# Optimization experiments

Hardware: AMD Instinct MI355X
Metric: run time of the kernel (lower is better)

The kernel has to match this reference:

```python
import jax, jax.numpy as jnp
import numpy as np

B, N, K, DIN, DM, DOUT = 4, 4096, 16, 256, 256, 256


def setup_inputs() -> dict:
    key = jax.random.key(0)
    ks = jax.random.split(key, 14)
    s = lambda k, shape: (jax.random.normal(k, shape, jnp.float32) * 0.02)
    return dict(
        xyz=jax.random.normal(ks[0], (B, N, 3), jnp.float32),
        features=jax.random.normal(ks[1], (B, N, DIN), jnp.float32),
        fc_delta_w1=s(ks[2], (3, DM)), fc_delta_b1=jnp.zeros((DM,), jnp.float32),
        fc_delta_w2=s(ks[3], (DM, DM)), fc_delta_b2=jnp.zeros((DM,), jnp.float32),
        fc1_w=s(ks[4], (DIN, DM)), fc1_b=jnp.zeros((DM,), jnp.float32),
        wq=s(ks[5], (DM, DM)), wk=s(ks[6], (DM, DM)), wv=s(ks[7], (DM, DM)),
        fc_gamma_w1=s(ks[8], (DM, DM)), fc_gamma_b1=jnp.zeros((DM,), jnp.float32),
        fc_gamma_w2=s(ks[9], (DM, DM)), fc_gamma_b2=jnp.zeros((DM,), jnp.float32),
        fc2_w=s(ks[10], (DM, DOUT)), fc2_b=jnp.zeros((DOUT,), jnp.float32),
        sc_w=s(ks[11], (DIN, DOUT)), sc_b=jnp.zeros((DOUT,), jnp.float32),
    )


def reference(xyz, features, fc_delta_w1, fc_delta_b1, fc_delta_w2, fc_delta_b2,
              fc1_w, fc1_b, wq, wk, wv, fc_gamma_w1, fc_gamma_b1,
              fc_gamma_w2, fc_gamma_b2, fc2_w, fc2_b, sc_w, sc_b):
    # kNN via squared euclidean distances (same ordering as cdist topk)
    x2 = jnp.sum(xyz * xyz, axis=-1)                                   # (B,N)
    d2 = x2[:, :, None] + x2[:, None, :] - 2.0 * jnp.einsum('bnd,bmd->bnm', xyz, xyz)
    knn_idx = jax.lax.top_k(-d2, K)[1]                                 # (B,N,K)

    gather = jax.vmap(lambda a, i: a[i])                               # per-batch gather
    knn_xyz = gather(xyz, knn_idx)                                     # (B,N,K,3)

    # positional encoding MLP on relative coordinates
    rel = xyz[:, :, None, :] - knn_xyz                                 # (B,N,K,3)
    pos_enc = jax.nn.relu(rel @ fc_delta_w1 + fc_delta_b1) @ fc_delta_w2 + fc_delta_b2

    shortcut = features
    f = features @ fc1_w + fc1_b                                       # (B,N,DM)
    knn_f = gather(f, knn_idx)                                         # (B,N,K,DM)

    q = f @ wq                                                         # (B,N,DM)
    k_ = knn_f @ wk                                                    # (B,N,K,DM)
    v = knn_f @ wv                                                     # (B,N,K,DM)

    a = q[:, :, None, :] - k_ + pos_enc                                # (B,N,K,DM)
    a = jax.nn.relu(a @ fc_gamma_w1 + fc_gamma_b1) @ fc_gamma_w2 + fc_gamma_b2
    attn = jax.nn.softmax(a / np.float32(np.sqrt(DM)), axis=-2)        # softmax over K

    res = jnp.einsum('bnkf,bnkf->bnf', attn, v + pos_enc)              # (B,N,DM)
    return res @ fc2_w + fc2_b + shortcut @ sc_w + sc_b                # (B,N,DOUT)
```

## Files before the change

### kernel.cpp

```cpp
#include <hip/hip_runtime.h>
#include <hip/hip_bf16.h>
#include <math.h>

typedef __attribute__((ext_vector_type(8))) short bf16x8;
typedef __attribute__((ext_vector_type(4))) float f32x4;
typedef __attribute__((ext_vector_type(4))) short s16x4;
typedef unsigned int u32;
typedef unsigned long long u64;

#define NBATCH 4
#define NPTS   4096
#define NTOT   (NBATCH*NPTS)
#define NROWS  (NTOT*16)

__device__ __forceinline__ float bf2f(unsigned short h){
  unsigned int u = ((unsigned int)h) << 16;
  return __builtin_bit_cast(float, u);
}
__device__ __forceinline__ unsigned short f2bf(float f){
  unsigned int u = __builtin_bit_cast(unsigned int, f);
  u += 0x7FFFu + ((u >> 16) & 1u);
  return (unsigned short)(u >> 16);
}
__device__ __forceinline__ unsigned short f2bfh(float f){
  return __bfloat16_as_ushort(__float2bfloat16(f));
}

#define MFMA(a,b,c) __builtin_amdgcn_mfma_f32_16x16x32_bf16((a),(b),(c),0,0,0)

typedef u32 __attribute__((address_space(1))) gas_u32;
typedef u32 __attribute__((address_space(3))) las_u32;
__device__ __forceinline__ void gl_lds16(const void* g, void* l){
  __builtin_amdgcn_global_load_lds((const gas_u32*)g, (las_u32*)l, 16, 0, 0);
}

__device__ __forceinline__ void wfence(){
  asm volatile("s_waitcnt lgkmcnt(0)" ::: "memory");
  __builtin_amdgcn_sched_barrier(0);
}

__global__ __launch_bounds__(256) void k_convert(const float* __restrict__ x,
                                                 unsigned short* __restrict__ xb, int n){
  int i = (blockIdx.x * 256 + threadIdx.x) * 4;
  if (i < n){
    float4 v = *(const float4*)(x + i);
    s16x4 o;
    o[0] = (short)f2bf(v.x); o[1] = (short)f2bf(v.y);
    o[2] = (short)f2bf(v.z); o[3] = (short)f2bf(v.w);
    *(s16x4*)(xb + i) = o;
  }
}

__global__ __launch_bounds__(256) void k_xyzw(const float* __restrict__ xyz,
                                              float4* __restrict__ xyzw){
  int i = blockIdx.x * 256 + threadIdx.x;
  float x = xyz[i*3], y = xyz[i*3+1], z = xyz[i*3+2];
  xyzw[i] = make_float4(x, y, z, x*x + y*y + z*z);
}

__global__ __launch_bounds__(256) void k_prep_mats(
    const float* __restrict__ scw, const float* __restrict__ g2,
    const float* __restrict__ fc2, const float* __restrict__ W2,
    const float* __restrict__ scb,
    unsigned short* __restrict__ qkv2T, unsigned short* __restrict__ g2sT,
    unsigned short* __restrict__ fc2T, unsigned short* __restrict__ BposT,
    float* __restrict__ cvec){
  int c = blockIdx.x, d = threadIdx.x;
  qkv2T[(768+c)*256 + d] = f2bf(scw[d*256 + c]);
  g2sT[c*256 + d]        = f2bf(g2[d*256 + c] * 0.0625f);
  fc2T[c*256 + d]        = f2bf(fc2[d*256 + c]);
  BposT[(256+c)*256 + d] = f2bf(W2[d*256 + c]);
  if (d == 0) cvec[768 + c] = scb[c];
}

__global__ __launch_bounds__(256) void k_prep_gemm(
    const float* __restrict__ wq, const float* __restrict__ wk,
    const float* __restrict__ g1, const float* __restrict__ W2,
    const float* __restrict__ b2d, const float* __restrict__ gb1,
    unsigned short* __restrict__ tmpWq, unsigned short* __restrict__ tmpWk,
    unsigned short* __restrict__ BposT, float* __restrict__ c1){
  int c = threadIdx.x, bid = blockIdx.x;
  if (bid < 256){
    int d = bid; float acc = 0.f;
    for (int e=0;e<256;e++) acc += wq[d*256+e]*g1[e*256+c];
    tmpWq[c*256 + d] = f2bf(acc);
  } else if (bid < 512){
    int d = bid-256; float acc = 0.f;
    for (int e=0;e<256;e++) acc += wk[d*256+e]*g1[e*256+c];
    tmpWk[c*256 + d] = f2bf(acc);
  } else if (bid < 768){
    int d = bid-512; float acc = 0.f;
    for (int e=0;e<256;e++) acc += W2[d*256+e]*g1[e*256+c];
    BposT[c*256 + d] = f2bf(acc);
  } else {
    float acc = 0.f;
    for (int e=0;e<256;e++) acc += b2d[e]*g1[e*256+c];
    c1[c] = acc + gb1[c];
  }
}

__global__ __launch_bounds__(256) void k_prep_gemm2(
    const float* __restrict__ fc1w, const float* __restrict__ fc1b,
    const float* __restrict__ wv,
    const unsigned short* __restrict__ tmpWq, const unsigned short* __restrict__ tmpWk,
    unsigned short* __restrict__ qkv2T, float* __restrict__ cvec){
  int c = threadIdx.x, bid = blockIdx.x;
  if (bid < 256){
    int d = bid; float acc = 0.f;
    for (int e=0;e<256;e++) acc += fc1w[d*256+e]*bf2f(tmpWq[c*256+e]);
    qkv2T[c*256 + d] = f2bf(acc);
  } else if (bid < 512){
    int d = bid-256; float acc = 0.f;
    for (int e=0;e<256;e++) acc += fc1w[d*256+e]*bf2f(tmpWk[c*256+e]);
    qkv2T[(256+c)*256 + d] = f2bf(acc);
  } else if (bid < 768){
    int d = bid-512; float acc = 0.f;
    for (int e=0;e<256;e++) acc += fc1w[d*256+e]*wv[e*256+c];
    qkv2T[(512+c)*256 + d] = f2bf(acc);
  } else {
    float aq=0.f, ak=0.f, av=0.f;
    for (int e=0;e<256;e++){
      float fb = fc1b[e];
      aq += fb*bf2f(tmpWq[c*256+e]);
      ak += fb*bf2f(tmpWk[c*256+e]);
      av += fb*wv[e*256+c];
    }
    cvec[c] = aq; cvec[256+c] = ak; cvec[512+c] = av;
  }
}

__device__ __forceinline__ u32 fmap(float d){
  u32 u = __builtin_bit_cast(u32, d);
  return ((int)u < 0) ? ~u : (u | 0x80000000u);
}

__device__ __forceinline__ void find_thresh(const int* hist, int lane, int need,
                                            int* e_out, int* c_out){
  int h0 = hist[lane*4], h1 = hist[lane*4+1], h2 = hist[lane*4+2], h3 = hist[lane*4+3];
  int ps = h0 + h1 + h2 + h3;
  int incl = ps;
  #pragma unroll
  for (int d = 1; d < 64; d <<= 1){
    int tv = __shfl_up(incl, d, 64);
    if (lane >= d) incl += tv;
  }
  int excl = incl - ps;
  int b0 = excl, b1 = excl + h0, b2 = b1 + h1, b3 = b2 + h2;
  bool f0 = (b0 < need) && (b0 + h0 >= need);
  bool f1 = (b1 < need) && (b1 + h1 >= need);
  bool f2 = (b2 < need) && (b2 + h2 >= need);
  bool f3 = (b3 < need) && (b3 + h3 >= need);
  int e_loc = f0 ? lane*4 : f1 ? lane*4+1 : f2 ? lane*4+2 : lane*4+3;
  int c_loc = f0 ? b0 : f1 ? b1 : f2 ? b2 : b3;
  u64 mk = __ballot(f0 | f1 | f2 | f3);
  int wl = __ffsll(mk) - 1;
  *e_out = __shfl(e_loc, wl, 64);
  *c_out = __shfl(c_loc, wl, 64);
}

__device__ __forceinline__ void find_thresh4(const int* hA, int lane, int need,
                                             int* e_out, int* c_out){
  int h[4];
  #pragma unroll
  for (int j=0;j<4;j++){
    int bin = lane*4+j;
    h[j] = hA[bin]
         + hA[256 + ((bin+8)&255)]
         + hA[512 + ((bin+16)&255)]
         + hA[768 + ((bin+24)&255)];
  }
  int ps = h[0] + h[1] + h[2] + h[3];
  int incl = ps;
  #pragma unroll
  for (int d = 1; d < 64; d <<= 1){
    int tv = __shfl_up(incl, d, 64);
    if (lane >= d) incl += tv;
  }
  int excl = incl - ps;
  int b0 = excl, b1 = excl + h[0], b2 = b1 + h[1], b3 = b2 + h[2];
  bool f0 = (b0 < need) && (b0 + h[0] >= need);
  bool f1 = (b1 < need) && (b1 + h[1] >= need);
  bool f2 = (b2 < need) && (b2 + h[2] >= need);
  bool f3 = (b3 < need) && (b3 + h[3] >= need);
  int e_loc = f0 ? lane*4 : f1 ? lane*4+1 : f2 ? lane*4+2 : lane*4+3;
  int c_loc = f0 ? b0 : f1 ? b1 : f2 ? b2 : b3;
  u64 mk = __ballot(f0 | f1 | f2 | f3);
  int wl = __ffsll(mk) - 1;
  *e_out = __shfl(e_loc, wl, 64);
  *c_out = __shfl(c_loc, wl, 64);
}

__global__ __launch_bounds__(256) void k_knn(const float4* __restrict__ xyzw,
                                             int* __restrict__ gidxbuf,
                                             float4* __restrict__ relbuf){
  __shared__ int histA[4][1024];
  __shared__ int histB[4][256];

  int t = threadIdx.x, lane = t & 63, wv = t >> 6;
  int widx = blockIdx.x * 4 + wv;
  int b = widx >> 12, n = widx & 4095;
  const float4* xb = xyzw + (size_t)b * NPTS;
  float4 P = xb[n];
  float x2n = P.w;
  int* hA = histA[wv]; int* hB = histB[wv];

  #pragma unroll
  for (int j = 0; j < 16; j++) hA[lane*16+j] = 0;
  #pragma unroll
  for (int j = 0; j < 4; j++)  hB[lane*4+j] = 0;
  wfence();

  int cp = lane >> 4;
  int cpoff = cp*256, cprot = cp*8;

  for (int it = 0; it < 64; it += 2){
    float4 Q0 = xb[it*64 + lane];
    float4 Q1 = xb[it*64 + 64 + lane];
    float d0 = x2n + Q0.w - 2.0f*(P.x*Q0.x + P.y*Q0.y + P.z*Q0.z);
    float d1 = x2n + Q1.w - 2.0f*(P.x*Q1.x + P.y*Q1.y + P.z*Q1.z);
    int b0 = (int)(fmap(d0) >> 24), b1 = (int)(fmap(d1) >> 24);
    atomicAdd(&hA[cpoff + ((b0 + cprot)&255)], 1);
    atomicAdd(&hA[cpoff + ((b1 + cprot)&255)], 1);
  }
  wfence();
  int e1, c0dummy;
  find_thresh4(hA, lane, 16, &e1, &c0dummy);
  wfence();

  u32* lstE_u = (u32*)&hA[0];
  int* lstE_m = &hA[128];
  u32* lstT_u = (u32*)&hA[256];
  int* lstT_m = &hA[320];

  int base = 0, Lc = 0;
  size_t orow = (size_t)widx * 16;
  for (int it = 0; it < 64; it++){
    int m = it*64 + lane;
    float4 Q = xb[m];
    u32 u = fmap(x2n + Q.w - 2.0f*(P.x*Q.x + P.y*Q.y + P.z*Q.z));
    int hi = (int)(u >> 24);
    bool def = hi < e1;
    bool bnd = hi == e1;
    u64 mkd = __ballot(def);
    if (def){
      int slot = base + __popcll(mkd & ((1ULL << lane) - 1ULL));
      gidxbuf[orow + slot] = b*NPTS + m;
      relbuf[orow + slot]  = make_float4(P.x - Q.x, P.y - Q.y, P.z - Q.z, 0.f);
    }
    base += __popcll(mkd);
    u64 mkb = __ballot(bnd);
    if (bnd){
      int sl = Lc + __popcll(mkb & ((1ULL << lane) - 1ULL));
      if (sl < 128){ lstE_u[sl] = u; lstE_m[sl] = m; }
      atomicAdd(&hB[(u >> 16) & 0xFF], 1);
    }
    Lc += __popcll(mkb);
  }
  wfence();
  int c0 = base;
  int m1, cc;
  find_thresh(hB, lane, 16 - c0, &m1, &cc);
  int c1 = c0 + cc;

  int nt = 0;
  if (Lc <= 128){
    int eb = c0;
    for (int ch = 0; ch < 128; ch += 64){
      int idx = ch + lane;
      bool valid = idx < Lc;
      u32 u = valid ? lstE_u[idx] : 0xFFFFFFFFu;
      int mid = valid ? (int)((u >> 16) & 0xFF) : 999;
      bool lt = valid && (mid < m1);
      u64 mk = __ballot(lt);
      if (lt){
        int slot = eb + __popcll(mk & ((1ULL << lane) - 1ULL));
        int m = lstE_m[idx];
        float4 Q = xb[m];
        gidxbuf[orow + slot] = b*NPTS + m;
        relbuf[orow + slot]  = make_float4(P.x - Q.x, P.y - Q.y, P.z - Q.z, 0.f);
      }
      eb += __popcll(mk);
      bool tie = valid && (mid == m1);
      u64 mkt = __ballot(tie);
      if (tie){
        int sl = nt + __popcll(mkt & ((1ULL << lane) - 1ULL));
        if (sl < 64){ lstT_u[sl] = u; lstT_m[sl] = lstE_m[idx]; }
      }
      nt += __popcll(mkt);
      if (Lc <= 64) break;
    }
  } else {
    int eb = c0;
    for (int it = 0; it < 64; it++){
      int m = it*64 + lane;
      float4 Q = xb[m];
      u32 u = fmap(x2n + Q.w - 2.0f*(P.x*Q.x + P.y*Q.y + P.z*Q.z));
      bool inb = ((int)(u >> 24) == e1);
      int mid = inb ? (int)((u >> 16) & 0xFF) : 999;
      bool lt = inb && (mid < m1);
      u64 mk = __ballot(lt);
      if (lt){
        int slot = eb + __popcll(mk & ((1ULL << lane) - 1ULL));
        gidxbuf[orow + slot] = b*NPTS + m;
        relbuf[orow + slot]  = make_float4(P.x - Q.x, P.y - Q.y, P.z - Q.z, 0.f);
      }
      eb += __popcll(mk);
      bool tie = inb && (mid == m1);
      u64 mkt = __ballot(tie);
      if (tie){
        int sl = nt + __popcll(mkt & ((1ULL << lane) - 1ULL));
        if (sl < 64){ lstT_u[sl] = u; lstT_m[sl] = m; }
      }
      nt += __popcll(mkt);
    }
  }
  wfence();
  if (nt > 64) nt = 64;

  int r2 = 16 - c1;
  u32 lu = (lane < nt) ? lstT_u[lane] : 0xFFFFFFFFu;
  int lm = (lane < nt) ? lstT_m[lane] : 0x7FFFFFFF;
  bool popped = false;
  for (int r = 0; r < r2; r++){
    u32 ku = popped ? 0xFFFFFFFFu : lu;
    int km = popped ? 0x7FFFFFFF : lm;
    #pragma unroll
    for (int off = 32; off >= 1; off >>= 1){
      u32 ou = __shfl_xor(ku, off, 64);
      int om = __shfl_xor(km, off, 64);
      if (ou < ku || (ou == ku && om < km)){ ku = ou; km = om; }
    }
    bool mine = !popped && (lane < nt) && (lu == ku) && (lm == km);
    u64 mk = __ballot(mine);
    int wl = __ffsll(mk) - 1;
    if (lane == wl){
      popped = true;
      float4 Q = xb[km];
      gidxbuf[orow + c1 + r] = b*NPTS + km;
      relbuf[orow + c1 + r]  = make_float4(P.x - Q.x, P.y - Q.y, P.z - Q.z, 0.f);
    }
  }
}

template<int MODE>
__global__ __launch_bounds__(512) void k_mm(
    const unsigned short* __restrict__ A, const unsigned short* __restrict__ BT,
    int rowbase,
    const float* __restrict__ bias, const float* __restrict__ b2v,
    const unsigned short* __restrict__ qg, const unsigned short* __restrict__ kg,
    const unsigned short* __restrict__ vb,
    const float4* __restrict__ relbuf, const int* __restrict__ gidxbuf,
    const float* __restrict__ W1, const float* __restrict__ b1d,
    unsigned short* __restrict__ o0, unsigned short* __restrict__ o1,
    unsigned short* __restrict__ o2, unsigned short* __restrict__ o3,
    const unsigned short* __restrict__ vper,
    float* __restrict__ fout){
  __shared__ unsigned short As[4096];
  __shared__ unsigned short Bs[8192];
  __shared__ float4 W1s4[256];
  __shared__ float4 relS[128];
  __shared__ int    gidxS[128];
  __shared__ float  biasS[256];

  int t = threadIdx.x;
  int lane = t & 63, w = t >> 6;
  int wm = w >> 2, wn = w & 3;
  int lrow = lane & 15, lkg = lane >> 4;
  int bx = blockIdx.x;
  if constexpr (MODE == 2){
    int gx = gridDim.x;
    bx = (bx & 7) * (gx >> 3) + (bx >> 3);
  }
  int m0 = bx * 128, n0 = blockIdx.y * 256;

  float4 rl0 = make_float4(0.f,0.f,0.f,0.f);
  if constexpr (MODE == 2){
    if (t < 128){
      relS[t]  = relbuf[(size_t)rowbase + m0 + t];
      gidxS[t] = gidxbuf[(size_t)rowbase + m0 + t];
    }
    if (t < 256){
      biasS[t] = (blockIdx.y == 0) ? bias[t] : b2v[t];
      W1s4[t] = make_float4(W1[t], W1[256+t], W1[512+t], b1d[t]);
    }
    __syncthreads();
    rl0 = relS[t >> 2];
  }
  if constexpr (MODE == 0){
    if (t < 256) biasS[t] = bias[n0 + t];
  }

  int sr = t >> 2, sc = (t & 3) * 8;
  unsigned short* lA  = As + (w << 9);
  unsigned short* lB  = Bs + (w << 9);
  unsigned short* lB2 = Bs + 4096 + (w << 9);
  const unsigned short* gB  = BT + (size_t)(n0 + sr)*256 + sc;
  const unsigned short* gB2 = BT + (size_t)(n0 + 128 + sr)*256 + sc;

  f32x4 acc[4][4] = {};
  for (int k0 = 0; k0 < 256; k0 += 32){
    if constexpr (MODE == 2){
      int r = t >> 2, h = (t & 3) << 3;
      bf16x8 h0;
      #pragma unroll
      for (int j = 0; j < 8; j++){
        int c = k0 + h + j;
        float4 wa = W1s4[c];
        float x0 = rl0.x*wa.x + rl0.y*wa.y + rl0.z*wa.z + wa.w;
        h0[j] = (short)f2bfh(fmaxf(x0, 0.f));
      }
      *(bf16x8*)&As[r*32 + h] = h0;
    } else {
      const unsigned short* gA = A + (size_t)(m0 + sr)*256 + k0 + sc;
      gl_lds16(gA, lA);
    }
    gl_lds16(gB  + k0, lB);
    gl_lds16(gB2 + k0, lB2);
    __syncthreads();
    bf16x8 af[4], bfr[4];
    #pragma unroll
    for (int fi = 0; fi < 4; fi++)
      af[fi] = *(const bf16x8*)&As[(wm*64 + fi*16 + lrow)*32 + lkg*8];
    #pragma unroll
    for (int nf = 0; nf < 4; nf++)
      bfr[nf] = *(const bf16x8*)&Bs[(wn*64 + nf*16 + lrow)*32 + lkg*8];
    #pragma unroll
    for (int fi = 0; fi < 4; fi++)
      #pragma unroll
      for (int nf = 0; nf < 4; nf++)
        acc[fi][nf] = MFMA(af[fi], bfr[nf], acc[fi][nf]);
    __syncthreads();
  }

  if constexpr (MODE == 0){
    unsigned short* outp = (blockIdx.y==0)?o0:(blockIdx.y==1)?o1:(blockIdx.y==2)?o2:o3;
    #pragma unroll
    for (int fi=0; fi<4; fi++)
      #pragma unroll
      for (int nf=0; nf<4; nf++)
        #pragma unroll
        for (int r=0;r<4;r++){
          int row = m0 + wm*64 + fi*16 + lkg*4 + r;
          int col = wn*64 + nf*16 + lrow;
          outp[(size_t)row*256 + col] = f2bf(acc[fi][nf][r] + biasS[col]);
        }
  } else if constexpr (MODE == 2){
    const bool is_a1 = (blockIdx.y == 0);
    #pragma unroll
    for (int fi=0; fi<4; fi++){
      int g = (rowbase + m0 + wm*64 + fi*16) >> 4;
      #pragma unroll
      for (int nf=0; nf<4; nf++){
        int colg = wn*64 + nf*16 + lrow;
        if (is_a1){
          float qv = bf2f(qg[(size_t)g*256 + colg]) + biasS[colg];
          #pragma unroll
          for (int r=0;r<4;r++){
            int rl_ = wm*64 + fi*16 + lkg*4 + r;
            int gi = gidxS[rl_];
            float a1 = acc[fi][nf][r] + qv - bf2f(kg[(size_t)gi*256 + colg]);
            o0[(size_t)(m0 + rl_)*256 + colg] = f2bfh(fmaxf(a1, 0.f));
          }
        } else {
          float bb = biasS[colg];
          #pragma unroll
          for (int r=0;r<4;r++){
            int rl_ = wm*64 + fi*16 + lkg*4 + r;
            int gi = gidxS[rl_];
            float vpe = acc[fi][nf][r] + bb + bf2f(vb[(size_t)gi*256 + colg]);
            o1[(size_t)(m0 + rl_)*256 + colg] = f2bfh(vpe);
          }
        }
      }
    }
  } else if constexpr (MODE == 3){
    #pragma unroll
    for (int fi=0; fi<4; fi++){
      int g = (rowbase + m0 + wm*64 + fi*16) >> 4;
      #pragma unroll
      for (int nf=0; nf<4; nf++){
        int colg = wn*64 + nf*16 + lrow;
        float s[4], e[4];
        #pragma unroll
        for (int r=0;r<4;r++) s[r] = acc[fi][nf][r] + bias[colg]*0.0625f;
        float mx = fmaxf(fmaxf(s[0],s[1]), fmaxf(s[2],s[3]));
        mx = fmaxf(mx, __shfl_xor(mx,16,64));
        mx = fmaxf(mx, __shfl_xor(mx,32,64));
        float sm = 0.f;
        #pragma unroll
        for (int r=0;r<4;r++){ e[r] = __expf(s[r]-mx); sm += e[r]; }
        sm += __shfl_xor(sm,16,64);
        sm += __shfl_xor(sm,32,64);
        float rs = 1.f/sm, tsum = 0.f;
        #pragma unroll
        for (int r=0;r<4;r++){
          int rl_ = wm*64 + fi*16 + lkg*4 + r;
          tsum += (e[r]*rs) * bf2f(vper[(size_t)(m0 + rl_)*256 + colg]);
        }
        tsum += __shfl_xor(tsum,16,64);
        tsum += __shfl_xor(tsum,32,64);
        if (lkg == 0) o0[(size_t)g*256 + colg] = f2bf(tsum);
      }
    }
  } else {
    #pragma unroll
    for (int fi=0; fi<4; fi++)
      #pragma unroll
      for (int nf=0; nf<4; nf++)
        #pragma unroll
        for (int r=0;r<4;r++){
          int row = m0 + wm*64 + fi*16 + lkg*4 + r;
          int col = wn*64 + nf*16 + lrow;
          fout[(size_t)row*256 + col] = acc[fi][nf][r] + bias[col]
                                      + bf2f(qg[(size_t)row*256 + col]);
        }
  }
}

extern "C" void kernel_launch(void* const* d_in, const int* in_sizes, int n_in,
                              void* d_out, int out_size, void* d_ws, size_t ws_size,
                              hipStream_t stream){
  (void)in_sizes; (void)n_in; (void)out_size;
  const float* xyz  = (const float*)d_in[0];
  const float* feat = (const float*)d_in[1];
  const float* W1   = (const float*)d_in[2];
  const float* b1d  = (const float*)d_in[3];
  const float* W2   = (const float*)d_in[4];
  const float* b2d  = (const float*)d_in[5];
  const float* fc1w = (const float*)d_in[6];
  const float* fc1b = (const float*)d_in[7];
  const float* wq   = (const float*)d_in[8];
  const float* wk   = (const float*)d_in[9];
  const float* wv   = (const float*)d_in[10];
  const float* g1   = (const float*)d_in[11];
  const float* gb1  = (const float*)d_in[12];
  const float* g2   = (const float*)d_in[13];
  const float* gb2  = (const float*)d_in[14];
  const float* fc2w = (const float*)d_in[15];
  const float* fc2b = (const float*)d_in[16];
  const float* scw  = (const float*)d_in[17];
  const float* scb  = (const float*)d_in[18];

  char* ws = (char*)d_ws;
  size_t off = 0;
  auto alloc = [&](size_t bytes)->void*{ void* p = ws + off; off += (bytes + 255) & ~(size_t)255; return p; };
  unsigned short* Xb     = (unsigned short*)alloc((size_t)NTOT*256*2);
  unsigned short* qgb    = (unsigned short*)alloc((size_t)NTOT*256*2);
  unsigned short* kgb    = (unsigned short*)alloc((size_t)NTOT*256*2);
  unsigned short* vbb    = (unsigned short*)alloc((size_t)NTOT*256*2);
  unsigned short* scbuf  = (unsigned short*)alloc((size_t)NTOT*256*2);
  int*            gidxbuf= (int*)alloc((size_t)NROWS*4);
  float4*         relbuf = (float4*)alloc((size_t)NROWS*16);
  float4*         xyzw   = (float4*)alloc((size_t)NTOT*16);
  unsigned short* qkv2T  = (unsigned short*)alloc(1024*256*2);
  unsigned short* tmpWq  = (unsigned short*)alloc(256*256*2);
  unsigned short* tmpWk  = (unsigned short*)alloc(256*256*2);
  unsigned short* BposT  = (unsigned short*)alloc(512*256*2);
  unsigned short* g2sT   = (unsigned short*)alloc(256*256*2);
  unsigned short* fc2T   = (unsigned short*)alloc(256*256*2);
  float*          c1     = (float*)alloc(256*4);
  float*          cvec   = (float*)alloc(1024*4);
  unsigned short* res    = Xb;

  int CR = NROWS;
  while (CR > 16384 && off + (size_t)CR*1024 > ws_size) CR >>= 1;
  unsigned short* a1buf  = (unsigned short*)alloc((size_t)CR*256*2);
  unsigned short* vpebuf = (unsigned short*)alloc((size_t)CR*256*2);

  k_convert<<<4096, 256, 0, stream>>>(feat, Xb, NTOT*256);
  k_xyzw<<<64, 256, 0, stream>>>(xyz, xyzw);
  k_prep_mats<<<256, 256, 0, stream>>>(scw, g2, fc2w, W2, scb, qkv2T, g2sT, fc2T, BposT, cvec);
  k_prep_gemm<<<769, 256, 0, stream>>>(wq, wk, g1, W2, b2d, gb1, tmpWq, tmpWk, BposT, c1);
  k_prep_gemm2<<<769, 256, 0, stream>>>(fc1w, fc1b, wv, tmpWq, tmpWk, qkv2T, cvec);
  k_knn<<<4096, 256, 0, stream>>>(xyzw, gidxbuf, relbuf);

  k_mm<0><<<dim3(128, 4), 512, 0, stream>>>(Xb, qkv2T, 0, cvec, nullptr,
      nullptr, nullptr, nullptr, nullptr, nullptr, nullptr, nullptr,
      qgb, kgb, vbb, scbuf, nullptr, nullptr);

  for (int c0 = 0; c0 < NROWS; c0 += CR){
    k_mm<2><<<dim3(CR/128, 2), 512, 0, stream>>>(nullptr, BposT, c0, c1, b2d,
        qgb, kgb, vbb, relbuf, gidxbuf, W1, b1d,
        a1buf, vpebuf, nullptr, nullptr, nullptr, nullptr);
    k_mm<3><<<dim3(CR/128, 1), 512, 0, stream>>>(a1buf, g2sT, c0, gb2, nullptr,
        nullptr, nullptr, nullptr, nullptr, nullptr, nullptr, nullptr,
        res, nullptr, nullptr, nullptr, vpebuf, nullptr);
  }

  k_mm<4><<<dim3(128, 1), 512, 0, stream>>>(res, fc2T, 0, fc2b, nullptr,
      scbuf, nullptr, nullptr, nullptr, nullptr, nullptr, nullptr,
      nullptr, nullptr, nullptr, nullptr, nullptr, (float*)d_out);
}
```

Measured before the change: 483.7 us.

## Fuse positional-encoding, gamma MLP, softmax and aggregation into one kernel

Replaces the MODE 2 and MODE 3 GEMM kernels, which wrote a1 and v+pos_enc intermediates to global memory, with a single fused kernel per 64-row tile. The a1 tile stays in swizzled LDS and feeds the gamma GEMM directly. Softmax weights stay in registers, and the v+pos_enc GEMM is recomputed and reduced on the fly, so the large bf16 intermediate buffers and their round trips are gone. The cost is more LDS per block (about 61 KB) and three accumulator sets, which may cut occupancy, plus recomputing the relu(rel*W1) A operand twice.

```diff
diff --git a/kernel.cpp b/kernel.cpp
--- a/kernel.cpp
+++ b/kernel.cpp
@@ -37,6 +37,10 @@
 __device__ __forceinline__ void wfence(){
   asm volatile("s_waitcnt lgkmcnt(0)" ::: "memory");
   __builtin_amdgcn_sched_barrier(0);
+}
+
+__device__ __forceinline__ unsigned int swz(int row, int kbyte){
+  return (unsigned int)(row * 512) + (((unsigned int)kbyte) ^ (((unsigned int)row & 7u) << 4));
 }
 
 __global__ __launch_bounds__(256) void k_convert(const float* __restrict__ x,
@@ -345,50 +349,20 @@
 template<int MODE>
 __global__ __launch_bounds__(512) void k_mm(
     const unsigned short* __restrict__ A, const unsigned short* __restrict__ BT,
-    int rowbase,
-    const float* __restrict__ bias, const float* __restrict__ b2v,
-    const unsigned short* __restrict__ qg, const unsigned short* __restrict__ kg,
-    const unsigned short* __restrict__ vb,
-    const float4* __restrict__ relbuf, const int* __restrict__ gidxbuf,
-    const float* __restrict__ W1, const float* __restrict__ b1d,
+    const float* __restrict__ bias,
     unsigned short* __restrict__ o0, unsigned short* __restrict__ o1,
     unsigned short* __restrict__ o2, unsigned short* __restrict__ o3,
-    const unsigned short* __restrict__ vper,
-    float* __restrict__ fout){
+    const unsigned short* __restrict__ scbuf, float* __restrict__ fout){
   __shared__ unsigned short As[4096];
   __shared__ unsigned short Bs[8192];
-  __shared__ float4 W1s4[256];
-  __shared__ float4 relS[128];
-  __shared__ int    gidxS[128];
   __shared__ float  biasS[256];
 
   int t = threadIdx.x;
   int lane = t & 63, w = t >> 6;
   int wm = w >> 2, wn = w & 3;
   int lrow = lane & 15, lkg = lane >> 4;
-  int bx = blockIdx.x;
-  if constexpr (MODE == 2){
-    int gx = gridDim.x;
-    bx = (bx & 7) * (gx >> 3) + (bx >> 3);
-  }
-  int m0 = bx * 128, n0 = blockIdx.y * 256;
-
-  float4 rl0 = make_float4(0.f,0.f,0.f,0.f);
-  if constexpr (MODE == 2){
-    if (t < 128){
-      relS[t]  = relbuf[(size_t)rowbase + m0 + t];
-      gidxS[t] = gidxbuf[(size_t)rowbase + m0 + t];
-    }
-    if (t < 256){
-      biasS[t] = (blockIdx.y == 0) ? bias[t] : b2v[t];
-      W1s4[t] = make_float4(W1[t], W1[256+t], W1[512+t], b1d[t]);
-    }
-    __syncthreads();
-    rl0 = relS[t >> 2];
-  }
-  if constexpr (MODE == 0){
-    if (t < 256) biasS[t] = bias[n0 + t];
-  }
+  int m0 = blockIdx.x * 128, n0 = blockIdx.y * 256;
+  if (t < 256) biasS[t] = bias[n0 + t];
 
   int sr = t >> 2, sc = (t & 3) * 8;
   unsigned short* lA  = As + (w << 9);
@@ -399,21 +373,8 @@
 
   f32x4 acc[4][4] = {};
   for (int k0 = 0; k0 < 256; k0 += 32){
-    if constexpr (MODE == 2){
-      int r = t >> 2, h = (t & 3) << 3;
-      bf16x8 h0;
-      #pragma unroll
-      for (int j = 0; j < 8; j++){
-        int c = k0 + h + j;
-        float4 wa = W1s4[c];
-        float x0 = rl0.x*wa.x + rl0.y*wa.y + rl0.z*wa.z + wa.w;
-        h0[j] = (short)f2bfh(fmaxf(x0, 0.f));
-      }
-      *(bf16x8*)&As[r*32 + h] = h0;
-    } else {
-      const unsigned short* gA = A + (size_t)(m0 + sr)*256 + k0 + sc;
-      gl_lds16(gA, lA);
-    }
+    const unsigned short* gA = A + (size_t)(m0 + sr)*256 + k0 + sc;
+    gl_lds16(gA, lA);
     gl_lds16(gB  + k0, lB);
     gl_lds16(gB2 + k0, lB2);
     __syncthreads();
@@ -444,64 +405,6 @@
           int col = wn*64 + nf*16 + lrow;
           outp[(size_t)row*256 + col] = f2bf(acc[fi][nf][r] + biasS[col]);
         }
-  } else if constexpr (MODE == 2){
-    const bool is_a1 = (blockIdx.y == 0);
-    #pragma unroll
-    for (int fi=0; fi<4; fi++){
-      int g = (rowbase + m0 + wm*64 + fi*16) >> 4;
-      #pragma unroll
-      for (int nf=0; nf<4; nf++){
-        int colg = wn*64 + nf*16 + lrow;
-        if (is_a1){
-          float qv = bf2f(qg[(size_t)g*256 + colg]) + biasS[colg];
-          #pragma unroll
-          for (int r=0;r<4;r++){
-            int rl_ = wm*64 + fi*16 + lkg*4 + r;
-            int gi = gidxS[rl_];
-            float a1 = acc[fi][nf][r] + qv - bf2f(kg[(size_t)gi*256 + colg]);
-            o0[(size_t)(m0 + rl_)*256 + colg] = f2bfh(fmaxf(a1, 0.f));
-          }
-        } else {
-          float bb = biasS[colg];
-          #pragma unroll
-          for (int r=0;r<4;r++){
-            int rl_ = wm*64 + fi*16 + lkg*4 + r;
-            int gi = gidxS[rl_];
-            float vpe = acc[fi][nf][r] + bb + bf2f(vb[(size_t)gi*256 + colg]);
-            o1[(size_t)(m0 + rl_)*256 + colg] = f2bfh(vpe);
-          }
-        }
-      }
-    }
-  } else if constexpr (MODE == 3){
-    #pragma unroll
-    for (int fi=0; fi<4; fi++){
-      int g = (rowbase + m0 + wm*64 + fi*16) >> 4;
-      #pragma unroll
-      for (int nf=0; nf<4; nf++){
-        int colg = wn*64 + nf*16 + lrow;
-        float s[4], e[4];
-        #pragma unroll
-        for (int r=0;r<4;r++) s[r] = acc[fi][nf][r] + bias[colg]*0.0625f;
-        float mx = fmaxf(fmaxf(s[0],s[1]), fmaxf(s[2],s[3]));
-        mx = fmaxf(mx, __shfl_xor(mx,16,64));
-        mx = fmaxf(mx, __shfl_xor(mx,32,64));
-        float sm = 0.f;
-        #pragma unroll
-        for (int r=0;r<4;r++){ e[r] = __expf(s[r]-mx); sm += e[r]; }
-        sm += __shfl_xor(sm,16,64);
-        sm += __shfl_xor(sm,32,64);
-        float rs = 1.f/sm, tsum = 0.f;
-        #pragma unroll
-        for (int r=0;r<4;r++){
-          int rl_ = wm*64 + fi*16 + lkg*4 + r;
-          tsum += (e[r]*rs) * bf2f(vper[(size_t)(m0 + rl_)*256 + colg]);
-        }
-        tsum += __shfl_xor(tsum,16,64);
-        tsum += __shfl_xor(tsum,32,64);
-        if (lkg == 0) o0[(size_t)g*256 + colg] = f2bf(tsum);
-      }
-    }
   } else {
     #pragma unroll
     for (int fi=0; fi<4; fi++)
@@ -511,16 +414,205 @@
         for (int r=0;r<4;r++){
           int row = m0 + wm*64 + fi*16 + lkg*4 + r;
           int col = wn*64 + nf*16 + lrow;
-          fout[(size_t)row*256 + col] = acc[fi][nf][r] + bias[col]
-                                      + bf2f(qg[(size_t)row*256 + col]);
+          fout[(size_t)row*256 + col] = acc[fi][nf][r] + biasS[col]
+                                      + bf2f(scbuf[(size_t)row*256 + col]);
         }
+  }
+}
+
+__global__ __launch_bounds__(256) void k_fused(
+    const unsigned short* __restrict__ BposT, const unsigned short* __restrict__ g2sT,
+    const unsigned short* __restrict__ qg, const unsigned short* __restrict__ kg,
+    const unsigned short* __restrict__ vb,
+    const float4* __restrict__ relbuf, const int* __restrict__ gidxbuf,
+    const float* __restrict__ W1, const float* __restrict__ b1d,
+    const float* __restrict__ c1, const float* __restrict__ b2d,
+    const float* __restrict__ gb2,
+    unsigned short* __restrict__ res){
+  extern __shared__ char smem[];
+  char*           a1sB  = smem;
+  unsigned short* As    = (unsigned short*)(smem + 32768);
+  unsigned short* Bs    = (unsigned short*)(smem + 36864);
+  float4*         W1s4  = (float4*)(smem + 53248);
+  float4*         relS  = (float4*)(smem + 57344);
+  int*            gidxS = (int*)(smem + 58368);
+  float*          c1s   = (float*)(smem + 58624);
+  float*          b2s   = (float*)(smem + 59648);
+  float*          gb2s  = (float*)(smem + 60672);
+
+  int t = threadIdx.x;
+  int lane = t & 63, w = t >> 6;
+  int wn = w;
+  int lrow = lane & 15, lkg = lane >> 4;
+  int bx = blockIdx.x;
+  { int gx = gridDim.x; bx = (bx & 7) * (gx >> 3) + (bx >> 3); }
+  int m0 = bx * 64;
+
+  if (t < 64){
+    relS[t]  = relbuf[(size_t)m0 + t];
+    gidxS[t] = gidxbuf[(size_t)m0 + t];
+  }
+  W1s4[t] = make_float4(W1[t], W1[256+t], W1[512+t], b1d[t]);
+  c1s[t] = c1[t]; b2s[t] = b2d[t]; gb2s[t] = gb2[t]*0.0625f;
+  __syncthreads();
+  float4 rl0 = relS[t >> 2];
+
+  int sr = t >> 2, sc = (t & 3) * 8;
+  unsigned short* lBq[4];
+  #pragma unroll
+  for (int q = 0; q < 4; q++) lBq[q] = Bs + q*2048 + w*512;
+
+  const unsigned short* BTa = BposT;
+  const unsigned short* BTb = g2sT;
+  const unsigned short* BTc = BposT + (size_t)256*256;
+
+  f32x4 acc[4][4] = {};
+  for (int k0 = 0; k0 < 256; k0 += 32){
+    {
+      int r = sr, h = (t & 3) << 3;
+      bf16x8 h0;
+      #pragma unroll
+      for (int j = 0; j < 8; j++){
+        int c = k0 + h + j;
+        float4 wa = W1s4[c];
+        float x0 = rl0.x*wa.x + rl0.y*wa.y + rl0.z*wa.z + wa.w;
+        h0[j] = (short)f2bfh(fmaxf(x0, 0.f));
+      }
+      *(bf16x8*)&As[r*32 + h] = h0;
+    }
+    #pragma unroll
+    for (int q = 0; q < 4; q++)
+      gl_lds16(BTa + (size_t)(q*64 + sr)*256 + k0 + sc, lBq[q]);
+    __syncthreads();
+    bf16x8 af[4], bfr[4];
+    #pragma unroll
+    for (int fi = 0; fi < 4; fi++)
+      af[fi] = *(const bf16x8*)&As[(fi*16 + lrow)*32 + lkg*8];
+    #pragma unroll
+    for (int nf = 0; nf < 4; nf++)
+      bfr[nf] = *(const bf16x8*)&Bs[(wn*64 + nf*16 + lrow)*32 + lkg*8];
+    #pragma unroll
+    for (int fi = 0; fi < 4; fi++)
+      #pragma unroll
+      for (int nf = 0; nf < 4; nf++)
+        acc[fi][nf] = MFMA(af[fi], bfr[nf], acc[fi][nf]);
+    __syncthreads();
+  }
+  #pragma unroll
+  for (int fi=0; fi<4; fi++){
+    int g = (m0 >> 4) + fi;
+    #pragma unroll
+    for (int nf=0; nf<4; nf++){
+      int colg = wn*64 + nf*16 + lrow;
+      float qv = bf2f(qg[(size_t)g*256 + colg]) + c1s[colg];
+      #pragma unroll
+      for (int r=0;r<4;r++){
+        int rl_ = fi*16 + lkg*4 + r;
+        float a1 = acc[fi][nf][r] + qv - bf2f(kg[(size_t)gidxS[rl_]*256 + colg]);
+        *(unsigned short*)(a1sB + swz(rl_, colg*2)) = f2bfh(fmaxf(a1, 0.f));
+      }
+    }
+  }
+  __syncthreads();
+
+  f32x4 acc3[4][4] = {};
+  for (int k0 = 0; k0 < 256; k0 += 32){
+    #pragma unroll
+    for (int q = 0; q < 4; q++)
+      gl_lds16(BTb + (size_t)(q*64 + sr)*256 + k0 + sc, lBq[q]);
+    __syncthreads();
+    bf16x8 af[4], bfr[4];
+    #pragma unroll
+    for (int fi = 0; fi < 4; fi++)
+      af[fi] = *(const bf16x8*)(a1sB + swz(fi*16 + lrow, k0*2 + lkg*16));
+    #pragma unroll
+    for (int nf = 0; nf < 4; nf++)
+      bfr[nf] = *(const bf16x8*)&Bs[(wn*64 + nf*16 + lrow)*32 + lkg*8];
+    #pragma unroll
+    for (int fi = 0; fi < 4; fi++)
+      #pragma unroll
+      for (int nf = 0; nf < 4; nf++)
+        acc3[fi][nf] = MFMA(af[fi], bfr[nf], acc3[fi][nf]);
+    __syncthreads();
+  }
+  #pragma unroll
+  for (int fi=0; fi<4; fi++)
+    #pragma unroll
+    for (int nf=0; nf<4; nf++){
+      int colg = wn*64 + nf*16 + lrow;
+      float s[4], e[4];
+      #pragma unroll
+      for (int r=0;r<4;r++) s[r] = acc3[fi][nf][r] + gb2s[colg];
+      float mx = fmaxf(fmaxf(s[0],s[1]), fmaxf(s[2],s[3]));
+      mx = fmaxf(mx, __shfl_xor(mx,16,64));
+      mx = fmaxf(mx, __shfl_xor(mx,32,64));
+      float sm = 0.f;
+      #pragma unroll
+      for (int r=0;r<4;r++){ e[r] = __expf(s[r]-mx); sm += e[r]; }
+      sm += __shfl_xor(sm,16,64);
+      sm += __shfl_xor(sm,32,64);
+      float rs = 1.f/sm;
+      #pragma unroll
+      for (int r=0;r<4;r++) acc3[fi][nf][r] = e[r]*rs;
+    }
+
+  f32x4 acc2[4][4] = {};
+  for (int k0 = 0; k0 < 256; k0 += 32){
+    {
+      int r = sr, h = (t & 3) << 3;
+      bf16x8 h0;
+      #pragma unroll
+      for (int j = 0; j < 8; j++){
+        int c = k0 + h + j;
+        float4 wa = W1s4[c];
+        float x0 = rl0.x*wa.x + rl0.y*wa.y + rl0.z*wa.z + wa.w;
+        h0[j] = (short)f2bfh(fmaxf(x0, 0.f));
+      }
+      *(bf16x8*)&As[r*32 + h] = h0;
+    }
+    #pragma unroll
+    for (int q = 0; q < 4; q++)
+      gl_lds16(BTc + (size_t)(q*64 + sr)*256 + k0 + sc, lBq[q]);
+    __syncthreads();
+    bf16x8 af[4], bfr[4];
+    #pragma unroll
+    for (int fi = 0; fi < 4; fi++)
+      af[fi] = *(const bf16x8*)&As[(fi*16 + lrow)*32 + lkg*8];
+    #pragma unroll
+    for (int nf = 0; nf < 4; nf++)
+      bfr[nf] = *(const bf16x8*)&Bs[(wn*64 + nf*16 + lrow)*32 + lkg*8];
+    #pragma unroll
+    for (int fi = 0; fi < 4; fi++)
+      #pragma unroll
+      for (int nf = 0; nf < 4; nf++)
+        acc2[fi][nf] = MFMA(af[fi], bfr[nf], acc2[fi][nf]);
+    __syncthreads();
+  }
+  #pragma unroll
+  for (int fi=0; fi<4; fi++){
+    int g = (m0 >> 4) + fi;
+    #pragma unroll
+    for (int nf=0; nf<4; nf++){
+      int colg = wn*64 + nf*16 + lrow;
+      float bb = b2s[colg];
+      float tsum = 0.f;
+      #pragma unroll
+      for (int r=0;r<4;r++){
+        int rl_ = fi*16 + lkg*4 + r;
+        float vv = acc2[fi][nf][r] + bb + bf2f(vb[(size_t)gidxS[rl_]*256 + colg]);
+        tsum += acc3[fi][nf][r] * vv;
+      }
+      tsum += __shfl_xor(tsum,16,64);
+      tsum += __shfl_xor(tsum,32,64);
+      if (lkg == 0) res[(size_t)g*256 + colg] = f2bf(tsum);
+    }
   }
 }
 
 extern "C" void kernel_launch(void* const* d_in, const int* in_sizes, int n_in,
                               void* d_out, int out_size, void* d_ws, size_t ws_size,
                               hipStream_t stream){
-  (void)in_sizes; (void)n_in; (void)out_size;
+  (void)in_sizes; (void)n_in; (void)out_size; (void)ws_size;
   const float* xyz  = (const float*)d_in[0];
   const float* feat = (const float*)d_in[1];
   const float* W1   = (const float*)d_in[2];
@@ -562,11 +654,6 @@
   float*          cvec   = (float*)alloc(1024*4);
   unsigned short* res    = Xb;
 
-  int CR = NROWS;
-  while (CR > 16384 && off + (size_t)CR*1024 > ws_size) CR >>= 1;
-  unsigned short* a1buf  = (unsigned short*)alloc((size_t)CR*256*2);
-  unsigned short* vpebuf = (unsigned short*)alloc((size_t)CR*256*2);
-
   k_convert<<<4096, 256, 0, stream>>>(feat, Xb, NTOT*256);
   k_xyzw<<<64, 256, 0, stream>>>(xyz, xyzw);
   k_prep_mats<<<256, 256, 0, stream>>>(scw, g2, fc2w, W2, scb, qkv2T, g2sT, fc2T, BposT, cvec);
@@ -574,20 +661,13 @@
   k_prep_gemm2<<<769, 256, 0, stream>>>(fc1w, fc1b, wv, tmpWq, tmpWk, qkv2T, cvec);
   k_knn<<<4096, 256, 0, stream>>>(xyzw, gidxbuf, relbuf);
 
-  k_mm<0><<<dim3(128, 4), 512, 0, stream>>>(Xb, qkv2T, 0, cvec, nullptr,
-      nullptr, nullptr, nullptr, nullptr, nullptr, nullptr, nullptr,
+  k_mm<0><<<dim3(128, 4), 512, 0, stream>>>(Xb, qkv2T, cvec,
       qgb, kgb, vbb, scbuf, nullptr, nullptr);
 
-  for (int c0 = 0; c0 < NROWS; c0 += CR){
-    k_mm<2><<<dim3(CR/128, 2), 512, 0, stream>>>(nullptr, BposT, c0, c1, b2d,
-        qgb, kgb, vbb, relbuf, gidxbuf, W1, b1d,
-        a1buf, vpebuf, nullptr, nullptr, nullptr, nullptr);
-    k_mm<3><<<dim3(CR/128, 1), 512, 0, stream>>>(a1buf, g2sT, c0, gb2, nullptr,
-        nullptr, nullptr, nullptr, nullptr, nullptr, nullptr, nullptr,
-        res, nullptr, nullptr, nullptr, vpebuf, nullptr);
-  }
-
-  k_mm<4><<<dim3(128, 1), 512, 0, stream>>>(res, fc2T, 0, fc2b, nullptr,
-      scbuf, nullptr, nullptr, nullptr, nullptr, nullptr, nullptr,
-      nullptr, nullptr, nullptr, nullptr, nullptr, (float*)d_out);
-}
+  hipFuncSetAttribute((const void*)k_fused, hipFuncAttributeMaxDynamicSharedMemorySize, 61696);
+  k_fused<<<dim3(NROWS/64), 256, 61696, stream>>>(BposT, g2sT, qgb, kgb, vbb,
+      relbuf, gidxbuf, W1, b1d, c1, b2d, gb2, res);
+
+  k_mm<4><<<dim3(128, 1), 512, 0, stream>>>(res, fc2T, fc2b,
+      nullptr, nullptr, nullptr, nullptr, scbuf, (float*)d_out);
+}
```

Result: faster. 439.3 us (median of 3 runs) (-9.2%).
